# Performance work log

Measured on AMD Instinct MI355X. Metric: run time of the kernel, lower is better.

## Reference

```python
import jax, jax.numpy as jnp
import numpy as np

N_NODES = 50000
N_EDGES = 1_600_000
IN_FEAT = 128
OUT_FEAT = 128
NUM_RELS = 16


def setup_inputs() -> dict:
    key = jax.random.key(0)
    k_h, k_w, k_src, k_dst, k_rel = jax.random.split(key, 5)
    h = jax.random.normal(k_h, (N_NODES, IN_FEAT), dtype=jnp.float32)
    # xavier_uniform with relu gain ~ sqrt(2) * sqrt(6/(in+out))
    gain = np.sqrt(2.0)
    bound = gain * np.sqrt(6.0 / (IN_FEAT + OUT_FEAT))
    weight = jax.random.uniform(k_w, (NUM_RELS, IN_FEAT, OUT_FEAT),
                                dtype=jnp.float32, minval=-bound, maxval=bound)
    bias = jnp.zeros((OUT_FEAT,), dtype=jnp.float32)
    src = jax.random.randint(k_src, (N_EDGES,), 0, N_NODES, dtype=jnp.int32)
    dst = jax.random.randint(k_dst, (N_EDGES,), 0, N_NODES, dtype=jnp.int32)
    rel_type = jax.random.randint(k_rel, (N_EDGES,), 0, NUM_RELS, dtype=jnp.int32)
    return {"h": h, "weight": weight, "bias": bias,
            "src": src, "dst": dst, "rel_type": rel_type}


def reference(h, weight, bias, src, dst, rel_type):
    # Transform every node by every relation weight once: [R, N, out]
    # (equivalent to per-edge bmm h[src] @ weight[rel], but avoids an
    #  [E, in, out] weight gather)
    hw = jnp.einsum('ni,rio->rno', h, weight)
    # Per-edge message: msg[e] = h[src[e]] @ weight[rel_type[e]]  -> [E, out]
    msg = hw[rel_type, src]
    # Scatter-sum aggregation to destination nodes: [N, out]
    agg = jax.ops.segment_sum(msg, dst, num_segments=h.shape[0])
    # apply_func: bias + relu
    out = jax.nn.relu(agg + bias)
    return out
```

## Files before the change

kernel.cpp:

```cpp
#include <hip/hip_runtime.h>
#include <hip/hip_bf16.h>
#include <stdint.h>

typedef __attribute__((ext_vector_type(8))) short short8_t;
typedef __attribute__((ext_vector_type(4))) float f32x4;
typedef __attribute__((ext_vector_type(4))) int   i32x4;

#define AS1 __attribute__((address_space(1)))
#define AS3 __attribute__((address_space(3)))

#define CB_SHIFT 9
#define CBUCK 512
#define FCHUNK 6144
#define PADSLACK 4096

__device__ __forceinline__ void gload_lds16(const void* g, void* l) {
    __builtin_amdgcn_global_load_lds((const AS1 unsigned int*)g,
                                     (AS3 unsigned int*)l, 16, 0, 0);
}

__device__ __forceinline__ unsigned short f2bf(float f) {
    unsigned int u = __float_as_uint(f);
    unsigned int r = (u + 0x7FFFu + ((u >> 16) & 1u)) >> 16;
    return (unsigned short)r;
}

__global__ void prep_kernel(const float* __restrict__ h,
                            unsigned short* __restrict__ hb,
                            const float* __restrict__ w,
                            unsigned short* __restrict__ wt,
                            const int* __restrict__ dst,
                            int* __restrict__ cnt,
                            unsigned int* __restrict__ zrow,
                            int total4, int total4p, int castBlocks,
                            int R, int nE, int nseg) {
    __shared__ int hist[128];
    const int b = blockIdx.x;
    if (b < castBlocks) {
        int t = b * 256 + threadIdx.x;
        if (t < total4) {
            float4 v = ((const float4*)h)[t];
            ushort4 o;
            o.x = f2bf(v.x); o.y = f2bf(v.y); o.z = f2bf(v.z); o.w = f2bf(v.w);
            *(ushort4*)(hb + (size_t)t * 4) = o;
        } else if (t < total4p) {
            *(ushort4*)(hb + (size_t)t * 4) = make_ushort4(0, 0, 0, 0);
        }
        return;
    }
    if (b < castBlocks + R) {
        int r = b - castBlocks;
        const float* wr = w + (size_t)r * 16384;
        unsigned short* wtr = wt + (size_t)r * 16384;
        for (int x = threadIdx.x; x < 16384; x += blockDim.x) {
            int i = x >> 7, o = x & 127;
            wtr[o * 128 + i] = f2bf(wr[x]);
        }
        return;
    }
    if (b < castBlocks + R + 256) {
        if (threadIdx.x < 128) hist[threadIdx.x] = 0;
        __syncthreads();
        int b2 = b - castBlocks - R;
        for (int e = b2 * 256 + threadIdx.x; e < nE; e += 65536)
            atomicAdd(&hist[dst[e] >> CB_SHIFT], 1);
        __syncthreads();
        if (threadIdx.x < nseg) {
            int v = hist[threadIdx.x];
            if (v) atomicAdd(cnt + threadIdx.x, v);
        }
        return;
    }
    if (threadIdx.x < 64) zrow[threadIdx.x] = 0u;
}

__global__ __launch_bounds__(512, 4) void gemm_kernel(
    const unsigned short* __restrict__ hb,
    const unsigned short* __restrict__ wt,
    unsigned short* __restrict__ hw,
    int r0, int rc, int np, int nwg)
{
    __shared__ __align__(16) char smem[65536];
    char* ldsA = smem;
    char* ldsB = smem + 32768;
    const int tid  = threadIdx.x;
    const int lane = tid & 63;
    const int wv   = tid >> 6;
    const int wr   = wv >> 1;
    const int wc   = wv & 1;
    const int l15  = lane & 15, kb = lane >> 4;

    const int flat = blockIdx.x;
    const int q = nwg >> 3, rm = nwg & 7;
    const int xcd = flat & 7, ii = flat >> 3;
    const int orig = (xcd < rm ? xcd * (q + 1) : rm * (q + 1) + (xcd - rm) * q) + ii;
    const int rloc = orig % rc;
    const int rowb = orig / rc;
    const int rel  = r0 + rloc;
    const size_t rowBase = (size_t)rowb * 128;

    const char* gA = (const char*)(hb + rowBase * 128);
    const char* gB = (const char*)(wt + (size_t)rel * 16384);

#pragma unroll
    for (int it = 0; it < 4; ++it) {
        int p = it * 8192 + tid * 16;
        int row = p >> 8;
        int so = (row << 8) + ((p & 255) ^ ((row & 7) << 4));
        gload_lds16(gA + so, ldsA + p);
        gload_lds16(gB + so, ldsB + p);
    }
    __syncthreads();

    f32x4 acc[2][4];
#pragma unroll
    for (int m = 0; m < 2; ++m)
#pragma unroll
        for (int n = 0; n < 4; ++n) acc[m][n] = (f32x4){0.f, 0.f, 0.f, 0.f};

#pragma unroll
    for (int kk = 0; kk < 4; ++kk) {
        short8_t a[2], b[4];
#pragma unroll
        for (int m = 0; m < 2; ++m) {
            int row = wr * 32 + m * 16 + l15;
            int byte = row * 256 + ((kk * 64 + kb * 16) ^ ((row & 7) << 4));
            a[m] = *(const short8_t*)(ldsA + byte);
        }
#pragma unroll
        for (int n = 0; n < 4; ++n) {
            int row = wc * 64 + n * 16 + l15;
            int byte = row * 256 + ((kk * 64 + kb * 16) ^ ((row & 7) << 4));
            b[n] = *(const short8_t*)(ldsB + byte);
        }
#pragma unroll
        for (int m = 0; m < 2; ++m)
#pragma unroll
            for (int n = 0; n < 4; ++n)
                acc[m][n] = __builtin_amdgcn_mfma_f32_16x16x32_bf16(
                    a[m], b[n], acc[m][n], 0, 0, 0);
    }

    __syncthreads();
#pragma unroll
    for (int m = 0; m < 2; ++m) {
#pragma unroll
        for (int n = 0; n < 4; ++n) {
            int col = wc * 64 + n * 16 + l15;
#pragma unroll
            for (int j = 0; j < 4; ++j) {
                int row = wr * 32 + m * 16 + kb * 4 + j;
                int byte = row * 256 + ((col * 2) ^ ((row & 7) << 4));
                *(unsigned short*)(smem + byte) = f2bf(acc[m][n][j]);
            }
        }
    }
    __syncthreads();

    char* gC = (char*)(hw + ((size_t)rloc * np + rowBase) * 128);
#pragma unroll
    for (int j = 0; j < 4; ++j) {
        int p = j * 8192 + tid * 16;
        int row = p >> 8;
        i32x4 v = *(const i32x4*)(smem + row * 256 + ((p & 255) ^ ((row & 7) << 4)));
        *(i32x4*)(gC + p) = v;
    }
}

__global__ __launch_bounds__(256) void fill_staged_kernel(
    const int* __restrict__ src, const int* __restrict__ dst,
    const int* __restrict__ rel, const int* __restrict__ cnt,
    int* __restrict__ cur,
    int* __restrict__ packed, int nE, int nseg, int np)
{
    __shared__ int stage[FCHUNK];
    __shared__ int hist[128], lscan[128], lcur[128], gbase[128], segb[128];
    const int tid = threadIdx.x;
    const int e0 = blockIdx.x * FCHUNK;
    const int e1 = min(nE, e0 + FCHUNK);

    if (tid < 128) {
        hist[tid] = 0;
        segb[tid] = (tid < nseg) ? cnt[tid] : 0;
    }
    __syncthreads();
    for (int off = 1; off < 128; off <<= 1) {
        int t = 0;
        if (tid < 128 && tid >= off) t = segb[tid - off];
        __syncthreads();
        if (tid < 128) segb[tid] += t;
        __syncthreads();
    }
    if (tid < 128) segb[tid] -= (tid < nseg) ? cnt[tid] : 0;

    for (int e = e0 + tid; e < e1; e += 256)
        atomicAdd(&hist[dst[e] >> CB_SHIFT], 1);
    __syncthreads();

    if (tid < 128) lscan[tid] = hist[tid];
    __syncthreads();
    for (int off = 1; off < 128; off <<= 1) {
        int t = 0;
        if (tid < 128 && tid >= off) t = lscan[tid - off];
        __syncthreads();
        if (tid < 128) lscan[tid] += t;
        __syncthreads();
    }
    if (tid < 128) {
        int excl = lscan[tid] - hist[tid];
        lcur[tid] = excl;
        lscan[tid] = excl;
        gbase[tid] = segb[tid] +
            ((tid < nseg && hist[tid]) ? atomicAdd(cur + tid, hist[tid]) : 0);
    }
    __syncthreads();

    for (int e = e0 + tid; e < e1; e += 256) {
        int d = dst[e];
        int seg = d >> CB_SHIFT;
        int pk = (rel[e] * np + src[e]) | ((d & (CBUCK - 1)) << 20);
        int lp = atomicAdd(&lcur[seg], 1);
        stage[lp] = pk;
    }
    __syncthreads();

    const int wv = tid >> 6, lane = tid & 63;
    for (int s = wv; s < nseg; s += 4) {
        int n = hist[s], from = lscan[s], to = gbase[s];
        for (int i = lane; i < n; i += 64)
            packed[to + i] = stage[from + i];
    }
}

__global__ __launch_bounds__(1024) void bin_kernel(
    const int* __restrict__ cnt,
    const int* __restrict__ packed,
    int* __restrict__ packed2,
    int2* __restrict__ s2e2,
    int nseg, int zrow)
{
    __shared__ int hist[CBUCK], pscn[CBUCK], cur[CBUCK];
    __shared__ int segb[128];
    const int b = blockIdx.x, tid = threadIdx.x;
    if (tid < 128) segb[tid] = (tid < nseg) ? cnt[tid] : 0;
    if (tid < CBUCK) hist[tid] = 0;
    __syncthreads();
    for (int off = 1; off < 128; off <<= 1) {
        int t = 0;
        if (tid < 128 && tid >= off) t = segb[tid - off];
        __syncthreads();
        if (tid < 128) segb[tid] += t;
        __syncthreads();
    }
    const int e0 = segb[b];
    const int s0 = e0 - cnt[b];
    for (int k = s0 + tid; k < e0; k += 1024)
        atomicAdd(&hist[(packed[k] >> 20) & (CBUCK - 1)], 1);
    __syncthreads();
    int pc = 0;
    if (tid < CBUCK) { pc = (hist[tid] + 7) & ~7; pscn[tid] = pc; }
    __syncthreads();
    for (int off = 1; off < CBUCK; off <<= 1) {
        int t = 0;
        if (tid < CBUCK && tid >= off) t = pscn[tid - off];
        __syncthreads();
        if (tid < CBUCK) pscn[tid] += t;
        __syncthreads();
    }
    int ps = 0;
    const int pbase = s0 + b * PADSLACK;
    if (tid < CBUCK) {
        ps = pbase + pscn[tid] - pc;
        cur[tid] = ps;
        s2e2[(size_t)b * CBUCK + tid] = make_int2(ps, ps + pc);
    }
    __syncthreads();
    for (int k = s0 + tid; k < e0; k += 1024) {
        int pk = packed[k];
        int pos = atomicAdd(&cur[(pk >> 20) & (CBUCK - 1)], 1);
        packed2[pos] = pk;
    }
    __syncthreads();
    if (tid < CBUCK) {
        int pend = ps + pc;
        for (int p = cur[tid]; p < pend; ++p) packed2[p] = zrow;
    }
}

__global__ __launch_bounds__(256) void gather2_kernel(
    const unsigned short* __restrict__ hw,
    const int2* __restrict__ s2e2,
    const int* __restrict__ packed2,
    const float* __restrict__ bias,
    float* __restrict__ outp, float* __restrict__ agg,
    int n, int r0np, int rcnp, int zrl, int flags )
{
    int wid  = (blockIdx.x * blockDim.x + threadIdx.x) >> 6;
    int lane = threadIdx.x & 63;
    if (wid >= n) return;
    int2 se = s2e2[wid];
    int s = se.x, e = se.y;
    float a0 = 0.f, a1 = 0.f, a2 = 0.f, a3 = 0.f;
    const uint2* hw8 = (const uint2*)hw;
    const int half = lane >> 5;
    const int c0 = lane & 31;

    for (int base = s; base < e; base += 64) {
        int m = e - base; if (m > 64) m = 64;
        int myp = (base + lane < e) ? packed2[base + lane] : 0;
        for (int k = 0; k < m; k += 8) {
            uint2 v[4];
#pragma unroll
            for (int t = 0; t < 4; ++t) {
                int pe = __shfl(myp, k + 2 * t + half);
                int rl = (pe & 0xFFFFF) - r0np;
                if ((unsigned)rl >= (unsigned)rcnp) rl = zrl;
                v[t] = hw8[(size_t)rl * 32 + c0];
            }
#pragma unroll
            for (int t = 0; t < 4; ++t) {
                a0 += __uint_as_float(v[t].x << 16);
                a1 += __uint_as_float(v[t].x & 0xFFFF0000u);
                a2 += __uint_as_float(v[t].y << 16);
                a3 += __uint_as_float(v[t].y & 0xFFFF0000u);
            }
        }
    }
    a0 += __shfl_xor(a0, 32);
    a1 += __shfl_xor(a1, 32);
    a2 += __shfl_xor(a2, 32);
    a3 += __shfl_xor(a3, 32);

    if (lane < 32) {
        float4 acc4 = make_float4(a0, a1, a2, a3);
        float* ap = agg + (size_t)wid * 128 + c0 * 4;
        if (!(flags & 1)) {
            float4 p = *(const float4*)ap;
            acc4.x += p.x; acc4.y += p.y; acc4.z += p.z; acc4.w += p.w;
        }
        if (flags & 2) {
            float4 bv = *(const float4*)(bias + c0 * 4);
            float4 o;
            o.x = fmaxf(acc4.x + bv.x, 0.f);
            o.y = fmaxf(acc4.y + bv.y, 0.f);
            o.z = fmaxf(acc4.z + bv.z, 0.f);
            o.w = fmaxf(acc4.w + bv.w, 0.f);
            *(float4*)(outp + (size_t)wid * 128 + c0 * 4) = o;
        } else {
            *(float4*)ap = acc4;
        }
    }
}

static inline size_t align256(size_t x) { return (x + 255) & ~(size_t)255; }

extern "C" void kernel_launch(void* const* d_in, const int* in_sizes, int n_in,
                              void* d_out, int out_size, void* d_ws, size_t ws_size,
                              hipStream_t stream) {
    const float* h    = (const float*)d_in[0];
    const float* w    = (const float*)d_in[1];
    const float* bias = (const float*)d_in[2];
    const int*   src  = (const int*)d_in[3];
    const int*   dst  = (const int*)d_in[4];
    const int*   rel  = (const int*)d_in[5];
    float* out = (float*)d_out;

    const int N  = in_sizes[0] / 128;
    const int E  = in_sizes[3];
    const int R  = in_sizes[1] / (128 * 128);
    const int NB = (N + 127) / 128;
    const int NP = NB * 128;
    const int NSEG = (N + CBUCK - 1) >> CB_SHIFT;

    char* ws = (char*)d_ws;
    size_t off = 0;
    unsigned short* hb = (unsigned short*)(ws + off);
    off = align256(off + (size_t)NP * 128 * 2);
    unsigned short* wt = (unsigned short*)(ws + off);
    off = align256(off + (size_t)R * 16384 * 2);
    int* cntA = (int*)(ws + off);
    off = align256(off + 128 * 4);
    int* curA = (int*)(ws + off);
    off = align256(off + 128 * 4);
    int2* s2e2A = (int2*)(ws + off);
    off = align256(off + (size_t)NSEG * CBUCK * 8);
    int* packed = (int*)(ws + off);
    off = align256(off + (size_t)E * 4);
    int* packed2 = (int*)(ws + off);
    off = align256(off + ((size_t)E + (size_t)NSEG * PADSLACK + 64) * 4);
    size_t fixed = off;

    size_t perRel = (size_t)NP * 128 * 2;
    size_t aggB   = (size_t)N * 128 * 4;
    size_t avail  = ws_size > fixed ? ws_size - fixed : 0;

    int RC, fused; float* agg; unsigned short* hwb;
    if (avail >= (size_t)R * perRel + 256) {
        RC = R; fused = 1;
        hwb = (unsigned short*)(ws + fixed);
        agg = (float*)(ws + fixed);
    } else {
        fused = 0;
        agg = (float*)(ws + fixed);
        size_t a2 = avail > aggB + 256 ? avail - aggB - 256 : 0;
        RC = (int)(a2 / perRel);
        if (RC > R) RC = R;
        if (RC < 1) RC = 1;
        hwb = (unsigned short*)(ws + align256(fixed + aggB));
    }

    hipMemsetAsync(cntA, 0, align256(128 * 4) + 128 * 4, stream);

    int total4  = N * 32;
    int total4p = NP * 32;
    int castBlocks = (total4p + 255) / 256;
    int prepBlocks = castBlocks + R + 256 + 1;
    prep_kernel<<<prepBlocks, 256, 0, stream>>>(
        h, hb, w, wt, dst, cntA,
        (unsigned int*)(hwb + (size_t)RC * NP * 128),
        total4, total4p, castBlocks, R, E, NSEG);

    fill_staged_kernel<<<(E + FCHUNK - 1) / FCHUNK, 256, 0, stream>>>(
        src, dst, rel, cntA, curA, packed, E, NSEG, NP);
    bin_kernel<<<NSEG, 1024, 0, stream>>>(cntA, packed, packed2, s2e2A,
                                          NSEG, R * NP);

    int gblocks = (N * 64 + 255) / 256;
    for (int r0 = 0; r0 < R; r0 += RC) {
        int rc = (R - r0 < RC) ? (R - r0) : RC;
        int nwg = NB * rc;
        gemm_kernel<<<nwg, 512, 0, stream>>>(hb, wt, hwb, r0, rc, NP, nwg);
        int flags = (r0 == 0 ? 1 : 0) | (r0 + rc >= R ? 2 : 0);
        gather2_kernel<<<gblocks, 256, 0, stream>>>(hwb, s2e2A, packed2, bias,
                                                    out, agg, N, r0 * NP,
                                                    rc * NP, RC * NP,
                                                    fused ? 3 : flags);
    }
}
```

Baseline: 215.3 us.

## Fuse edge binning into first GEMM launch as extra blocks

```diff
diff --git a/kernel.cpp b/kernel.cpp
--- a/kernel.cpp
+++ b/kernel.cpp
@@ -74,23 +74,73 @@
     if (threadIdx.x < 64) zrow[threadIdx.x] = 0u;
 }
 
-__global__ __launch_bounds__(512, 4) void gemm_kernel(
+__global__ __launch_bounds__(512, 4) void binGemm_kernel(
+    const int* __restrict__ cnt, const int* __restrict__ packed,
+    int* __restrict__ packed2, int2* __restrict__ s2e2,
+    int nseg, int zrow, int binBlocks,
     const unsigned short* __restrict__ hb,
     const unsigned short* __restrict__ wt,
     unsigned short* __restrict__ hw,
     int r0, int rc, int np, int nwg)
 {
     __shared__ __align__(16) char smem[65536];
+    const int tid = threadIdx.x;
+
+    if (blockIdx.x < (unsigned)binBlocks) {
+        int* hist = (int*)smem;
+        int* pscn = hist + CBUCK;
+        int* cur  = pscn + CBUCK;
+        int* segb = cur + CBUCK;
+        const int b = blockIdx.x;
+        if (tid < 128) segb[tid] = (tid < nseg) ? cnt[tid] : 0;
+        hist[tid] = 0;
+        __syncthreads();
+        for (int off = 1; off < 128; off <<= 1) {
+            int t = 0;
+            if (tid < 128 && tid >= off) t = segb[tid - off];
+            __syncthreads();
+            if (tid < 128) segb[tid] += t;
+            __syncthreads();
+        }
+        const int e0 = segb[b];
+        const int s0 = e0 - cnt[b];
+        for (int k = s0 + tid; k < e0; k += 512)
+            atomicAdd(&hist[(packed[k] >> 20) & (CBUCK - 1)], 1);
+        __syncthreads();
+        int pc = (hist[tid] + 7) & ~7;
+        pscn[tid] = pc;
+        __syncthreads();
+        for (int off = 1; off < CBUCK; off <<= 1) {
+            int t = (tid >= off) ? pscn[tid - off] : 0;
+            __syncthreads();
+            pscn[tid] += t;
+            __syncthreads();
+        }
+        const int pbase = s0 + b * PADSLACK;
+        int ps = pbase + pscn[tid] - pc;
+        cur[tid] = ps;
+        s2e2[(size_t)b * CBUCK + tid] = make_int2(ps, ps + pc);
+        __syncthreads();
+        for (int k = s0 + tid; k < e0; k += 512) {
+            int pk = packed[k];
+            int pos = atomicAdd(&cur[(pk >> 20) & (CBUCK - 1)], 1);
+            packed2[pos] = pk;
+        }
+        __syncthreads();
+        int pend = ps + pc;
+        for (int p = cur[tid]; p < pend; ++p) packed2[p] = zrow;
+        return;
+    }
+
     char* ldsA = smem;
     char* ldsB = smem + 32768;
-    const int tid  = threadIdx.x;
     const int lane = tid & 63;
     const int wv   = tid >> 6;
     const int wr   = wv >> 1;
     const int wc   = wv & 1;
     const int l15  = lane & 15, kb = lane >> 4;
 
-    const int flat = blockIdx.x;
+    const int flat = blockIdx.x - binBlocks;
     const int q = nwg >> 3, rm = nwg & 7;
     const int xcd = flat & 7, ii = flat >> 3;
     const int orig = (xcd < rm ? xcd * (q + 1) : rm * (q + 1) + (xcd - rm) * q) + ii;
@@ -229,61 +279,6 @@
         int n = hist[s], from = lscan[s], to = gbase[s];
         for (int i = lane; i < n; i += 64)
             packed[to + i] = stage[from + i];
-    }
-}
-
-__global__ __launch_bounds__(1024) void bin_kernel(
-    const int* __restrict__ cnt,
-    const int* __restrict__ packed,
-    int* __restrict__ packed2,
-    int2* __restrict__ s2e2,
-    int nseg, int zrow)
-{
-    __shared__ int hist[CBUCK], pscn[CBUCK], cur[CBUCK];
-    __shared__ int segb[128];
-    const int b = blockIdx.x, tid = threadIdx.x;
-    if (tid < 128) segb[tid] = (tid < nseg) ? cnt[tid] : 0;
-    if (tid < CBUCK) hist[tid] = 0;
-    __syncthreads();
-    for (int off = 1; off < 128; off <<= 1) {
-        int t = 0;
-        if (tid < 128 && tid >= off) t = segb[tid - off];
-        __syncthreads();
-        if (tid < 128) segb[tid] += t;
-        __syncthreads();
-    }
-    const int e0 = segb[b];
-    const int s0 = e0 - cnt[b];
-    for (int k = s0 + tid; k < e0; k += 1024)
-        atomicAdd(&hist[(packed[k] >> 20) & (CBUCK - 1)], 1);
-    __syncthreads();
-    int pc = 0;
-    if (tid < CBUCK) { pc = (hist[tid] + 7) & ~7; pscn[tid] = pc; }
-    __syncthreads();
-    for (int off = 1; off < CBUCK; off <<= 1) {
-        int t = 0;
-        if (tid < CBUCK && tid >= off) t = pscn[tid - off];
-        __syncthreads();
-        if (tid < CBUCK) pscn[tid] += t;
-        __syncthreads();
-    }
-    int ps = 0;
-    const int pbase = s0 + b * PADSLACK;
-    if (tid < CBUCK) {
-        ps = pbase + pscn[tid] - pc;
-        cur[tid] = ps;
-        s2e2[(size_t)b * CBUCK + tid] = make_int2(ps, ps + pc);
-    }
-    __syncthreads();
-    for (int k = s0 + tid; k < e0; k += 1024) {
-        int pk = packed[k];
-        int pos = atomicAdd(&cur[(pk >> 20) & (CBUCK - 1)], 1);
-        packed2[pos] = pk;
-    }
-    __syncthreads();
-    if (tid < CBUCK) {
-        int pend = ps + pc;
-        for (int p = cur[tid]; p < pend; ++p) packed2[p] = zrow;
     }
 }
 
@@ -422,14 +417,15 @@
 
     fill_staged_kernel<<<(E + FCHUNK - 1) / FCHUNK, 256, 0, stream>>>(
         src, dst, rel, cntA, curA, packed, E, NSEG, NP);
-    bin_kernel<<<NSEG, 1024, 0, stream>>>(cntA, packed, packed2, s2e2A,
-                                          NSEG, R * NP);
 
     int gblocks = (N * 64 + 255) / 256;
     for (int r0 = 0; r0 < R; r0 += RC) {
         int rc = (R - r0 < RC) ? (R - r0) : RC;
         int nwg = NB * rc;
-        gemm_kernel<<<nwg, 512, 0, stream>>>(hb, wt, hwb, r0, rc, NP, nwg);
+        int binBlocks = (r0 == 0) ? NSEG : 0;
+        binGemm_kernel<<<binBlocks + nwg, 512, 0, stream>>>(
+            cntA, packed, packed2, s2e2A, NSEG, R * NP, binBlocks,
+            hb, wt, hwb, r0, rc, NP, nwg);
         int flags = (r0 == 0 ? 1 : 0) | (r0 + rc >= R ? 2 : 0);
         gather2_kernel<<<gblocks, 256, 0, stream>>>(hwb, s2e2A, packed2, bias,
                                                     out, agg, N, r0 * NP,
```

New measurement: 202.1 us. -6.2%, faster.
